# Optimization experiments

Hardware: AMD Instinct MI355X
Metric: run time of the kernel (lower is better)

Reference implementation:

```python
import jax, jax.numpy as jnp
import numpy as np

N = 4096
F_IN = 512
F_OUT = 64
HEADS = 8
ALPHA = 0.2  # LeakyReLU negative slope
NEG_INF = -9e15


def setup_inputs() -> dict:
    key = jax.random.key(0)
    k1, k2, k3, k4 = jax.random.split(key, 4)
    x = jax.random.normal(k1, (N, F_IN), dtype=jnp.float32)
    adj = jax.random.randint(k2, (N, N), 0, 2, dtype=jnp.int32)  # dense 0/1 adjacency
    # xavier_uniform with gain=1.414 per head
    limW = 1.414 * float(np.sqrt(6.0 / (F_IN + F_OUT)))
    lima = 1.414 * float(np.sqrt(6.0 / (2 * F_OUT + 1)))
    W = jax.random.uniform(k3, (HEADS, F_IN, F_OUT), minval=-limW, maxval=limW, dtype=jnp.float32)
    a = jax.random.uniform(k4, (HEADS, 2 * F_OUT), minval=-lima, maxval=lima, dtype=jnp.float32)
    return {"x": x, "adj": adj, "W": W, "a": a}


def reference(x, adj, W, a):
    # Per-head linear: Wh [H, N, F_OUT]
    Wh = jnp.einsum("nf,hfo->hno", x, W)
    # Pairwise concat + matmul with a decomposes into f1_i + f2_j
    f1 = jnp.einsum("hno,ho->hn", Wh, a[:, :F_OUT])  # [H, N]
    f2 = jnp.einsum("hno,ho->hn", Wh, a[:, F_OUT:])  # [H, N]
    e = jax.nn.leaky_relu(f1[:, :, None] + f2[:, None, :], ALPHA)  # [H, N, N]
    e = jnp.where(adj[None, :, :] > 0, e, NEG_INF)
    attn = jax.nn.softmax(e, axis=-1)  # masked row softmax; dropout is eval-mode identity
    out = jnp.einsum("hnm,hmo->hno", attn, Wh)  # weighted aggregation
    # concat heads: [N, H*F_OUT]
    return jnp.transpose(out, (1, 0, 2)).reshape(N, HEADS * F_OUT)
```

## Files before the change

### kernel.cpp

```cpp
#include <hip/hip_runtime.h>

#define NN   4096
#define FIN  512
#define FOUT 64
#define NH   8
#define ALPHA 0.2f
#define ROWS 128

typedef __attribute__((ext_vector_type(8))) short bf16x8;
typedef __attribute__((ext_vector_type(4))) float f32x4;

__device__ __forceinline__ unsigned short f2bf(float x) {
    unsigned u = __float_as_uint(x);
    return (unsigned short)((u + 0x7fffu + ((u >> 16) & 1u)) >> 16);
}

__global__ __launch_bounds__(256) void kb(const int* __restrict__ adj,
                                          unsigned long long* __restrict__ bits) {
    const int wv   = blockIdx.x * 4 + (threadIdx.x >> 6);
    const int lane = threadIdx.x & 63;
    const int base = wv * 32;
    #pragma unroll
    for (int r = 0; r < 4; ++r) {
        int v0 = adj[(size_t)(base + r*8 + 0) * 64 + lane];
        int v1 = adj[(size_t)(base + r*8 + 1) * 64 + lane];
        int v2 = adj[(size_t)(base + r*8 + 2) * 64 + lane];
        int v3 = adj[(size_t)(base + r*8 + 3) * 64 + lane];
        int v4 = adj[(size_t)(base + r*8 + 4) * 64 + lane];
        int v5 = adj[(size_t)(base + r*8 + 5) * 64 + lane];
        int v6 = adj[(size_t)(base + r*8 + 6) * 64 + lane];
        int v7 = adj[(size_t)(base + r*8 + 7) * 64 + lane];
        unsigned long long m0 = __ballot(v0 > 0);
        unsigned long long m1 = __ballot(v1 > 0);
        unsigned long long m2 = __ballot(v2 > 0);
        unsigned long long m3 = __ballot(v3 > 0);
        unsigned long long m4 = __ballot(v4 > 0);
        unsigned long long m5 = __ballot(v5 > 0);
        unsigned long long m6 = __ballot(v6 > 0);
        unsigned long long m7 = __ballot(v7 > 0);
        if (lane == 0) {
            ulonglong2* dst = (ulonglong2*)&bits[base + r*8];
            dst[0] = {m0, m1};
            dst[1] = {m2, m3};
            dst[2] = {m4, m5};
            dst[3] = {m6, m7};
        }
    }
}

__global__ __launch_bounds__(256) void kg(const float* __restrict__ x,
                                          const float* __restrict__ W,
                                          const float* __restrict__ aw,
                                          unsigned short* __restrict__ WhTs,
                                          float* __restrict__ f1,
                                          float* __restrict__ f2) {
    __shared__ float As[16][68];
    __shared__ float Bs[16][68];
    __shared__ unsigned short Tb[64][80];
    __shared__ float r1[64][16];
    __shared__ float r2[64][16];
    const int t = threadIdx.x;
    const int bx   = blockIdx.x;
    const int h    = bx >> 6;
    const int nti  = bx & 63;
    const int row0 = nti * 64;
    const int tr = t >> 4, tc = t & 15;
    const int ar = t >> 2, ak = t & 3;
    const int bk = t >> 4, bo = t & 15;
    const float* WH = W + (size_t)h * FIN * FOUT;
    float acc[4][4] = {};

    for (int k0i = 0; k0i < FIN; k0i += 16) {
        __syncthreads();
        float4 av = *(const float4*)&x[(size_t)(row0 + ar) * FIN + k0i + ak * 4];
        As[ak*4+0][ar] = av.x; As[ak*4+1][ar] = av.y;
        As[ak*4+2][ar] = av.z; As[ak*4+3][ar] = av.w;
        *(float4*)&Bs[bk][bo*4] =
            *(const float4*)&WH[(size_t)(k0i + bk) * FOUT + bo*4];
        __syncthreads();
        #pragma unroll
        for (int kk = 0; kk < 16; ++kk) {
            float4 a4 = *(const float4*)&As[kk][tr*4];
            float4 b4 = *(const float4*)&Bs[kk][tc*4];
            float a[4] = {a4.x, a4.y, a4.z, a4.w};
            float b[4] = {b4.x, b4.y, b4.z, b4.w};
            #pragma unroll
            for (int i = 0; i < 4; ++i)
                #pragma unroll
                for (int j = 0; j < 4; ++j)
                    acc[i][j] = fmaf(a[i], b[j], acc[i][j]);
        }
    }

    float a1v[4], a2v[4];
    #pragma unroll
    for (int j = 0; j < 4; ++j) {
        a1v[j] = aw[h * 2 * FOUT + tc*4 + j];
        a2v[j] = aw[h * 2 * FOUT + FOUT + tc*4 + j];
    }
    #pragma unroll
    for (int i = 0; i < 4; ++i) {
        float s1 = 0.f, s2 = 0.f;
        #pragma unroll
        for (int j = 0; j < 4; ++j) {
            s1 = fmaf(acc[i][j], a1v[j], s1);
            s2 = fmaf(acc[i][j], a2v[j], s2);
            Tb[tc*4 + j][tr*4 + i] = f2bf(acc[i][j]);
        }
        r1[tr*4 + i][tc] = s1;
        r2[tr*4 + i][tc] = s2;
    }
    __syncthreads();
    if (t < 64) {
        float s1 = 0.f, s2 = 0.f;
        #pragma unroll
        for (int k = 0; k < 16; ++k) { s1 += r1[t][k]; s2 += r2[t][k]; }
        f1[h * NN + row0 + t] = s1;
        f2[h * NN + row0 + t] = s2;
    }
    unsigned char* tileB = (unsigned char*)(WhTs + ((size_t)(h * 64) + nti) * 4096);
    #pragma unroll
    for (int i = 0; i < 2; ++i) {
        int c = t + i * 256;
        int o = c >> 3, nch = c & 7;
        *(uint4*)(tileB + o * 128 + ((nch * 16) ^ ((o & 7) << 4))) =
            *(const uint4*)&Tb[o][nch * 8];
    }
}

__global__ __launch_bounds__(256, 4) void k3_attn(
        const unsigned long long* __restrict__ bits,
        const unsigned short* __restrict__ WhTs,
        const float* __restrict__ f1, const float* __restrict__ f2,
        float* __restrict__ pnum, float* __restrict__ pden) {
    __shared__ unsigned char psB[ROWS * 128];
    __shared__ unsigned char wsB[8192];
    __shared__ float dred[ROWS][2];
    const int t    = threadIdx.x;
    const int lane = t & 63, wid = t >> 6;
    const int h    = blockIdx.y;
    const int row0 = blockIdx.x * ROWS;
    const int js   = blockIdx.z, JS = gridDim.z;
    const int ntile = (NN / 64) / JS;
    const int nt0   = js * ntile;
    const int pr   = t >> 1, psub = t & 1;
    const float f1r = f1[h * NN + row0 + pr];
    const float* f2h = f2 + h * NN;
    const unsigned long long* bitsRow = bits + (size_t)(row0 + pr) * 64;
    const unsigned short* WTS = WhTs + (size_t)h * 64 * 4096;
    const int prswz = (pr & 7) << 4;
    f32x4 acc[2][4] = {};
    float dsum = 0.f;

    uint4 wreg0, wreg1;
    auto loadW = [&](int nti, uint4& w0, uint4& w1) {
        const uint4* gt = (const uint4*)(WTS + (size_t)nti * 4096);
        w0 = gt[t];
        w1 = gt[t + 256];
    };
    loadW(nt0, wreg0, wreg1);

    const int kb2 = (lane >> 4) * 16;
    for (int it = 0; it < ntile; ++it) {
        const int nti = nt0 + it;
        __syncthreads();
        *(uint4*)&wsB[t * 16]        = wreg0;
        *(uint4*)&wsB[t * 16 + 4096] = wreg1;
        {
            unsigned msk = (unsigned)(bitsRow[nti] >> (psub << 5));
            const float* f2c = f2h + nti * 64 + psub * 32;
            #pragma unroll
            for (int q = 0; q < 4; ++q) {
                unsigned pk[4];
                #pragma unroll
                for (int c2 = 0; c2 < 2; ++c2) {
                    float4 f4 = *(const float4*)&f2c[q * 8 + c2 * 4];
                    float e0 = f1r + f4.x, e1 = f1r + f4.y;
                    float e2 = f1r + f4.z, e3 = f1r + f4.w;
                    e0 = fmaxf(e0, ALPHA * e0); e1 = fmaxf(e1, ALPHA * e1);
                    e2 = fmaxf(e2, ALPHA * e2); e3 = fmaxf(e3, ALPHA * e3);
                    const int b = q * 8 + c2 * 4;
                    float p0 = ((msk >> (b+0)) & 1u) ? __expf(e0) : 0.f;
                    float p1 = ((msk >> (b+1)) & 1u) ? __expf(e1) : 0.f;
                    float p2 = ((msk >> (b+2)) & 1u) ? __expf(e2) : 0.f;
                    float p3 = ((msk >> (b+3)) & 1u) ? __expf(e3) : 0.f;
                    dsum += (p0 + p1) + (p2 + p3);
                    pk[c2*2+0] = (unsigned)f2bf(p0) | ((unsigned)f2bf(p1) << 16);
                    pk[c2*2+1] = (unsigned)f2bf(p2) | ((unsigned)f2bf(p3) << 16);
                }
                uint4 w = {pk[0], pk[1], pk[2], pk[3]};
                *(uint4*)&psB[pr * 128 + ((psub*64 + q*16) ^ prswz)] = w;
            }
        }
        if (it + 1 < ntile) loadW(nti + 1, wreg0, wreg1);
        __syncthreads();
        #pragma unroll
        for (int fg = 0; fg < 2; ++fg) {
            const int arw  = wid * 32 + fg * 16 + (lane & 15);
            const int aswz = (arw & 7) << 4;
            #pragma unroll
            for (int ks = 0; ks < 2; ++ks) {
                bf16x8 af = *(const bf16x8*)&psB[arw * 128 + ((ks*64 + kb2) ^ aswz)];
                #pragma unroll
                for (int cf = 0; cf < 4; ++cf) {
                    int brw = cf * 16 + (lane & 15);
                    bf16x8 bfr = *(const bf16x8*)&wsB[brw * 128 + ((ks*64 + kb2) ^ ((brw & 7) << 4))];
                    acc[fg][cf] = __builtin_amdgcn_mfma_f32_16x16x32_bf16(af, bfr, acc[fg][cf], 0, 0, 0);
                }
            }
        }
    }

    dred[pr][psub] = dsum;
    __syncthreads();

    float* pn = pnum + (((size_t)js * NH + h) * NN + row0) * 64;
    #pragma unroll
    for (int fg = 0; fg < 2; ++fg)
        #pragma unroll
        for (int cf = 0; cf < 4; ++cf) {
            int o = cf * 16 + (lane & 15);
            #pragma unroll
            for (int rg = 0; rg < 4; ++rg) {
                int rl = wid * 32 + fg * 16 + (lane >> 4) * 4 + rg;
                pn[(size_t)rl * 64 + o] = acc[fg][cf][rg];
            }
        }
    if (t < ROWS)
        pden[((size_t)js * NH + h) * NN + row0 + t] = dred[t][0] + dred[t][1];
}

__global__ __launch_bounds__(256) void k4_red(const float* __restrict__ pnum,
                                              const float* __restrict__ pden,
                                              float* __restrict__ out, int JS) {
    const int idx = blockIdx.x * 256 + threadIdx.x;
    const int h   = idx >> 16;
    const int rem = idx & 65535;
    const int n   = rem >> 4;
    const int o4  = (rem & 15) * 4;
    float4 s = {0.f, 0.f, 0.f, 0.f};
    float  d = 0.f;
    for (int js = 0; js < JS; ++js) {
        const float* p = pnum + (((size_t)js * NH + h) * NN + n) * 64 + o4;
        float4 v = *(const float4*)p;
        s.x += v.x; s.y += v.y; s.z += v.z; s.w += v.w;
        d += pden[((size_t)js * NH + h) * NN + n];
    }
    float inv = 1.0f / d;
    float4 r = {s.x * inv, s.y * inv, s.z * inv, s.w * inv};
    *(float4*)&out[(size_t)n * (NH * FOUT) + h * FOUT + o4] = r;
}

extern "C" void kernel_launch(void* const* d_in, const int* in_sizes, int n_in,
                              void* d_out, int out_size, void* d_ws, size_t ws_size,
                              hipStream_t stream) {
    const float* x   = (const float*)d_in[0];
    const int*   adj = (const int*)d_in[1];
    const float* W   = (const float*)d_in[2];
    const float* a   = (const float*)d_in[3];
    float* outp = (float*)d_out;

    unsigned short* WhTs = (unsigned short*)d_ws;
    float* f1 = (float*)(WhTs + (size_t)NH * 64 * NN);
    float* f2 = f1 + NH * NN;
    unsigned long long* bits = (unsigned long long*)(f2 + NH * NN);
    float* pnum = (float*)(bits + (size_t)NN * 64);
    const size_t baseBytes  = (size_t)(pnum - (float*)d_ws) * 4;
    const size_t sliceBytes = (size_t)NH * NN * 65 * 4;
    int JS = 1;
    if (ws_size >= baseBytes + 4 * sliceBytes) JS = 4;
    else if (ws_size >= baseBytes + 2 * sliceBytes) JS = 2;
    float* pden = pnum + (size_t)JS * NH * NN * 64;

    kb     <<<dim3(2048),            256, 0, stream>>>(adj, bits);
    kg     <<<dim3(512),             256, 0, stream>>>(x, W, a, WhTs, f1, f2);
    k3_attn<<<dim3(NN/ROWS, NH, JS), 256, 0, stream>>>(bits, WhTs, f1, f2, pnum, pden);
    k4_red <<<dim3(NN*NH*FOUT/4/256), 256, 0, stream>>>(pnum, pden, outp, JS);
}
```

Baseline: 116.2 us.

## Merge bitmask and projection kernels; use exp2 and MFMA for softmax denominators

Fuses the adjacency bit-packing kernel and the Wh projection kernel into one launch, with block ranges split by index, to cut a launch and let the two independent jobs overlap. Pre-scales f1/f2 by log2(e) so the attention loop can use the hardware exp2 builtin directly. Computes the row denominators with an extra MFMA against a ones vector instead of scalar accumulation plus an LDS reduction and barrier, and packs bf16 pairs with the library conversion. The denominator now sums the bf16-rounded probabilities, so it matches the numerator's rounding, and the fused kernel still allocates the GEMM's shared memory for the bitmask blocks.

New measurement: 115.9 us. About the same (-0.3%).

```diff
diff --git a/kernel.cpp b/kernel.cpp
--- a/kernel.cpp
+++ b/kernel.cpp
@@ -1,4 +1,5 @@
 #include <hip/hip_runtime.h>
+#include <hip/hip_bf16.h>
 
 #define NN   4096
 #define FIN  512
@@ -6,6 +7,7 @@
 #define NH   8
 #define ALPHA 0.2f
 #define ROWS 128
+#define LOG2E 1.4426950408889634f
 
 typedef __attribute__((ext_vector_type(8))) short bf16x8;
 typedef __attribute__((ext_vector_type(4))) float f32x4;
@@ -15,52 +17,63 @@
     return (unsigned short)((u + 0x7fffu + ((u >> 16) & 1u)) >> 16);
 }
 
-__global__ __launch_bounds__(256) void kb(const int* __restrict__ adj,
-                                          unsigned long long* __restrict__ bits) {
-    const int wv   = blockIdx.x * 4 + (threadIdx.x >> 6);
-    const int lane = threadIdx.x & 63;
-    const int base = wv * 32;
-    #pragma unroll
-    for (int r = 0; r < 4; ++r) {
-        int v0 = adj[(size_t)(base + r*8 + 0) * 64 + lane];
-        int v1 = adj[(size_t)(base + r*8 + 1) * 64 + lane];
-        int v2 = adj[(size_t)(base + r*8 + 2) * 64 + lane];
-        int v3 = adj[(size_t)(base + r*8 + 3) * 64 + lane];
-        int v4 = adj[(size_t)(base + r*8 + 4) * 64 + lane];
-        int v5 = adj[(size_t)(base + r*8 + 5) * 64 + lane];
-        int v6 = adj[(size_t)(base + r*8 + 6) * 64 + lane];
-        int v7 = adj[(size_t)(base + r*8 + 7) * 64 + lane];
-        unsigned long long m0 = __ballot(v0 > 0);
-        unsigned long long m1 = __ballot(v1 > 0);
-        unsigned long long m2 = __ballot(v2 > 0);
-        unsigned long long m3 = __ballot(v3 > 0);
-        unsigned long long m4 = __ballot(v4 > 0);
-        unsigned long long m5 = __ballot(v5 > 0);
-        unsigned long long m6 = __ballot(v6 > 0);
-        unsigned long long m7 = __ballot(v7 > 0);
-        if (lane == 0) {
-            ulonglong2* dst = (ulonglong2*)&bits[base + r*8];
-            dst[0] = {m0, m1};
-            dst[1] = {m2, m3};
-            dst[2] = {m4, m5};
-            dst[3] = {m6, m7};
-        }
-    }
-}
-
-__global__ __launch_bounds__(256) void kg(const float* __restrict__ x,
-                                          const float* __restrict__ W,
-                                          const float* __restrict__ aw,
-                                          unsigned short* __restrict__ WhTs,
-                                          float* __restrict__ f1,
-                                          float* __restrict__ f2) {
+__device__ __forceinline__ unsigned pk2(float a, float b) {
+    union { __hip_bfloat162 h2; unsigned u; } cv;
+    cv.h2 = __float22bfloat162_rn(float2{a, b});
+    return cv.u;
+}
+
+#define BITB 2048
+
+__global__ __launch_bounds__(256) void kbg(const float* __restrict__ x,
+                                           const int*   __restrict__ adj,
+                                           const float* __restrict__ W,
+                                           const float* __restrict__ aw,
+                                           unsigned long long* __restrict__ bits,
+                                           unsigned short* __restrict__ WhTs,
+                                           float* __restrict__ f1,
+                                           float* __restrict__ f2) {
     __shared__ float As[16][68];
     __shared__ float Bs[16][68];
     __shared__ unsigned short Tb[64][80];
     __shared__ float r1[64][16];
     __shared__ float r2[64][16];
     const int t = threadIdx.x;
-    const int bx   = blockIdx.x;
+
+    if (blockIdx.x < BITB) {
+        const int wv   = blockIdx.x * 4 + (t >> 6);
+        const int lane = t & 63;
+        const int base = wv * 32;
+        #pragma unroll
+        for (int r = 0; r < 4; ++r) {
+            int v0 = adj[(size_t)(base + r*8 + 0) * 64 + lane];
+            int v1 = adj[(size_t)(base + r*8 + 1) * 64 + lane];
+            int v2 = adj[(size_t)(base + r*8 + 2) * 64 + lane];
+            int v3 = adj[(size_t)(base + r*8 + 3) * 64 + lane];
+            int v4 = adj[(size_t)(base + r*8 + 4) * 64 + lane];
+            int v5 = adj[(size_t)(base + r*8 + 5) * 64 + lane];
+            int v6 = adj[(size_t)(base + r*8 + 6) * 64 + lane];
+            int v7 = adj[(size_t)(base + r*8 + 7) * 64 + lane];
+            unsigned long long m0 = __ballot(v0 > 0);
+            unsigned long long m1 = __ballot(v1 > 0);
+            unsigned long long m2 = __ballot(v2 > 0);
+            unsigned long long m3 = __ballot(v3 > 0);
+            unsigned long long m4 = __ballot(v4 > 0);
+            unsigned long long m5 = __ballot(v5 > 0);
+            unsigned long long m6 = __ballot(v6 > 0);
+            unsigned long long m7 = __ballot(v7 > 0);
+            if (lane == 0) {
+                ulonglong2* dst = (ulonglong2*)&bits[base + r*8];
+                dst[0] = {m0, m1};
+                dst[1] = {m2, m3};
+                dst[2] = {m4, m5};
+                dst[3] = {m6, m7};
+            }
+        }
+        return;
+    }
+
+    const int bx   = blockIdx.x - BITB;
     const int h    = bx >> 6;
     const int nti  = bx & 63;
     const int row0 = nti * 64;
@@ -115,8 +128,8 @@
         float s1 = 0.f, s2 = 0.f;
         #pragma unroll
         for (int k = 0; k < 16; ++k) { s1 += r1[t][k]; s2 += r2[t][k]; }
-        f1[h * NN + row0 + t] = s1;
-        f2[h * NN + row0 + t] = s2;
+        f1[h * NN + row0 + t] = s1 * LOG2E;
+        f2[h * NN + row0 + t] = s2 * LOG2E;
     }
     unsigned char* tileB = (unsigned char*)(WhTs + ((size_t)(h * 64) + nti) * 4096);
     #pragma unroll
@@ -135,7 +148,6 @@
         float* __restrict__ pnum, float* __restrict__ pden) {
     __shared__ unsigned char psB[ROWS * 128];
     __shared__ unsigned char wsB[8192];
-    __shared__ float dred[ROWS][2];
     const int t    = threadIdx.x;
     const int lane = t & 63, wid = t >> 6;
     const int h    = blockIdx.y;
@@ -150,7 +162,9 @@
     const unsigned short* WTS = WhTs + (size_t)h * 64 * 4096;
     const int prswz = (pr & 7) << 4;
     f32x4 acc[2][4] = {};
-    float dsum = 0.f;
+    f32x4 accd[2] = {};
+    const bf16x8 ones = {0x3F80, 0x3F80, 0x3F80, 0x3F80,
+                         0x3F80, 0x3F80, 0x3F80, 0x3F80};
 
     uint4 wreg0, wreg1;
     auto loadW = [&](int nti, uint4& w0, uint4& w1) {
@@ -180,13 +194,12 @@
                     e0 = fmaxf(e0, ALPHA * e0); e1 = fmaxf(e1, ALPHA * e1);
                     e2 = fmaxf(e2, ALPHA * e2); e3 = fmaxf(e3, ALPHA * e3);
                     const int b = q * 8 + c2 * 4;
-                    float p0 = ((msk >> (b+0)) & 1u) ? __expf(e0) : 0.f;
-                    float p1 = ((msk >> (b+1)) & 1u) ? __expf(e1) : 0.f;
-                    float p2 = ((msk >> (b+2)) & 1u) ? __expf(e2) : 0.f;
-                    float p3 = ((msk >> (b+3)) & 1u) ? __expf(e3) : 0.f;
-                    dsum += (p0 + p1) + (p2 + p3);
-                    pk[c2*2+0] = (unsigned)f2bf(p0) | ((unsigned)f2bf(p1) << 16);
-                    pk[c2*2+1] = (unsigned)f2bf(p2) | ((unsigned)f2bf(p3) << 16);
+                    float p0 = ((msk >> (b+0)) & 1u) ? __builtin_amdgcn_exp2f(e0) : 0.f;
+                    float p1 = ((msk >> (b+1)) & 1u) ? __builtin_amdgcn_exp2f(e1) : 0.f;
+                    float p2 = ((msk >> (b+2)) & 1u) ? __builtin_amdgcn_exp2f(e2) : 0.f;
+                    float p3 = ((msk >> (b+3)) & 1u) ? __builtin_amdgcn_exp2f(e3) : 0.f;
+                    pk[c2*2+0] = pk2(p0, p1);
+                    pk[c2*2+1] = pk2(p2, p3);
                 }
                 uint4 w = {pk[0], pk[1], pk[2], pk[3]};
                 *(uint4*)&psB[pr * 128 + ((psub*64 + q*16) ^ prswz)] = w;
@@ -201,6 +214,7 @@
             #pragma unroll
             for (int ks = 0; ks < 2; ++ks) {
                 bf16x8 af = *(const bf16x8*)&psB[arw * 128 + ((ks*64 + kb2) ^ aswz)];
+                accd[fg] = __builtin_amdgcn_mfma_f32_16x16x32_bf16(af, ones, accd[fg], 0, 0, 0);
                 #pragma unroll
                 for (int cf = 0; cf < 4; ++cf) {
                     int brw = cf * 16 + (lane & 15);
@@ -211,9 +225,6 @@
         }
     }
 
-    dred[pr][psub] = dsum;
-    __syncthreads();
-
     float* pn = pnum + (((size_t)js * NH + h) * NN + row0) * 64;
     #pragma unroll
     for (int fg = 0; fg < 2; ++fg)
@@ -226,8 +237,14 @@
                 pn[(size_t)rl * 64 + o] = acc[fg][cf][rg];
             }
         }
-    if (t < ROWS)
-        pden[((size_t)js * NH + h) * NN + row0 + t] = dred[t][0] + dred[t][1];
+    if ((lane & 15) == 0) {
+        float* pd = pden + ((size_t)js * NH + h) * NN + row0;
+        #pragma unroll
+        for (int fg = 0; fg < 2; ++fg)
+            #pragma unroll
+            for (int rg = 0; rg < 4; ++rg)
+                pd[wid * 32 + fg * 16 + (lane >> 4) * 4 + rg] = accd[fg][rg];
+    }
 }
 
 __global__ __launch_bounds__(256) void k4_red(const float* __restrict__ pnum,
@@ -272,8 +289,7 @@
     else if (ws_size >= baseBytes + 2 * sliceBytes) JS = 2;
     float* pden = pnum + (size_t)JS * NH * NN * 64;
 
-    kb     <<<dim3(2048),            256, 0, stream>>>(adj, bits);
-    kg     <<<dim3(512),             256, 0, stream>>>(x, W, a, WhTs, f1, f2);
+    kbg    <<<dim3(BITB + 512),      256, 0, stream>>>(x, adj, W, a, bits, WhTs, f1, f2);
     k3_attn<<<dim3(NN/ROWS, NH, JS), 256, 0, stream>>>(bits, WhTs, f1, f2, pnum, pden);
     k4_red <<<dim3(NN*NH*FOUT/4/256), 256, 0, stream>>>(pnum, pden, outp, JS);
 }
```
